# Kernel tuning notes

Hardware: AMD Instinct MI355X
Metric: run time of the kernel (lower is better)

The kernel has to match this reference:

```python
import jax, jax.numpy as jnp
import numpy as np
import math
from jax import lax

TSCALE = 256
NUM_SAMPLE = 32
PERBIN = 3
WINDOWS = [4, 8, 16, 32, 64, 128, 192, 256]
RATIO = 0.25
B = 2
DIM = 512
H1 = 256   # hid_dim_1d
H3 = 512   # hid_dim_3d
H2 = 128   # hid_dim_2d


def _bin_mask(xmin, xmax, tscale, num_sample, perbin):
    # exact replica of BEM._get_interp1d_bin_mask (setup-time numpy)
    plen = float(xmax - xmin)
    step = plen / (num_sample * perbin - 1.0)
    samples = [xmin + step * i for i in range(num_sample * perbin)]
    cols = []
    for idx in range(num_sample):
        v = np.zeros([tscale])
        for s in samples[idx * perbin:(idx + 1) * perbin]:
            up = math.ceil(s)
            dec, down = math.modf(s)
            if 0 <= int(down) <= tscale - 1:
                v[int(down)] += 1 - dec
            if 0 <= int(up) <= tscale - 1:
                v[int(up)] += dec
        cols.append(v / perbin)
    return np.stack(cols, axis=1)  # (tscale, num_sample)


def build_sample_mask():
    mats = []
    for w in WINDOWS:
        ws = w + w * RATIO
        vecs = []
        for t in range(TSCALE):
            d = ws * 0.5
            vecs.append(_bin_mask(t - d, t + d, TSCALE, NUM_SAMPLE, PERBIN))
        mats.append(np.stack(vecs, axis=2))  # (T, N, T)
    m = np.stack(mats, axis=3).astype(np.float32)  # (T, N, T, W)
    return jnp.asarray(m.reshape(TSCALE, -1))  # (T, N*T*W)


def gn(x, g, b, groups=32, eps=1e-5):
    Bsz, C = x.shape[0], x.shape[1]
    xr = x.reshape(Bsz, groups, -1)
    mu = xr.mean(-1, keepdims=True)
    var = xr.var(-1, keepdims=True)
    xr = (xr - mu) * lax.rsqrt(var + eps)
    x = xr.reshape(x.shape)
    bshape = (1, C) + (1,) * (x.ndim - 2)
    return x * g.reshape(bshape) + b.reshape(bshape)


def conv(x, w, b, strides, padding, dn):
    y = lax.conv_general_dilated(x, w, strides, padding, dimension_numbers=dn)
    return y + b.reshape((1, -1) + (1,) * (y.ndim - 2))


def setup_inputs() -> dict:
    key = jax.random.key(0)
    ks = jax.random.split(key, 16)

    def w(k, shape, fan):
        return (jax.random.normal(k, shape) * (1.0 / np.sqrt(fan))).astype(jnp.float32)

    inp = {}
    inp['x'] = jax.random.normal(ks[0], (B, DIM, TSCALE), jnp.float32)
    inp['sample_mask'] = build_sample_mask()
    inp['c1_w'] = w(ks[1], (H1, DIM, 3), DIM * 3)
    inp['c1_b'] = jnp.zeros((H1,), jnp.float32)
    inp['gn1_g'] = jnp.ones((H1,), jnp.float32)
    inp['gn1_b'] = jnp.zeros((H1,), jnp.float32)
    inp['r3d_w'] = w(ks[2], (H3, H1, NUM_SAMPLE, 1, 1), H1 * NUM_SAMPLE)
    inp['r3d_b'] = jnp.zeros((H3,), jnp.float32)
    inp['gn3_g'] = jnp.ones((H3,), jnp.float32)
    inp['gn3_b'] = jnp.zeros((H3,), jnp.float32)
    inp['r2d_w'] = w(ks[3], (H2, H3, 1, 1), H3)
    inp['r2d_b'] = jnp.zeros((H2,), jnp.float32)
    inp['gn2_g'] = jnp.ones((H2,), jnp.float32)
    inp['gn2_b'] = jnp.zeros((H2,), jnp.float32)
    inp['s1_w'] = w(ks[4], (H2, H2, 3, 3), H2 * 9)
    inp['s1_b'] = jnp.zeros((H2,), jnp.float32)
    inp['sgn_g'] = jnp.ones((H2,), jnp.float32)
    inp['sgn_b'] = jnp.zeros((H2,), jnp.float32)
    inp['s2_w'] = w(ks[5], (1, H2, 1, 1), H2)
    inp['s2_b'] = jnp.zeros((1,), jnp.float32)
    inp['e1_w'] = w(ks[6], (H2, H2, 3, 3), H2 * 9)
    inp['e1_b'] = jnp.zeros((H2,), jnp.float32)
    inp['egn_g'] = jnp.ones((H2,), jnp.float32)
    inp['egn_b'] = jnp.zeros((H2,), jnp.float32)
    inp['e2_w'] = w(ks[7], (1, H2, 1, 1), H2)
    inp['e2_b'] = jnp.zeros((1,), jnp.float32)
    return inp


def reference(x, sample_mask, c1_w, c1_b, gn1_g, gn1_b, r3d_w, r3d_b, gn3_g, gn3_b,
              r2d_w, r2d_b, gn2_g, gn2_b, s1_w, s1_b, sgn_g, sgn_b, s2_w, s2_b,
              e1_w, e1_b, egn_g, egn_b, e2_w, e2_b):
    relu = jax.nn.relu
    W = len(WINDOWS)
    # conv_1: Unit1D(k=3, same pad) + GN + ReLU  -> (B, H1, T)
    h = relu(gn(conv(x, c1_w, c1_b, (1,), [(1, 1)], ('NCH', 'OIH', 'NCH')), gn1_g, gn1_b))
    Bsz, C, T = h.shape
    # sample: dense GEMM against sparse interp1d mask -> (B, C, N, T, W)
    samp = jnp.matmul(h, sample_mask).reshape(Bsz, C, NUM_SAMPLE, T, W)
    # reduction_layer 'fc': Conv3d over the N axis (kernel=stride=N) + GN + ReLU
    y = conv(samp, r3d_w, r3d_b, (NUM_SAMPLE, 1, 1), 'VALID', ('NCDHW', 'OIDHW', 'NCDHW'))
    y = relu(gn(y, gn3_g, gn3_b))[:, :, 0]  # squeeze depth -> (B, H3, T, W)
    f = relu(gn(conv(y, r2d_w, r2d_b, (1, 1), 'VALID', ('NCHW', 'OIHW', 'NCHW')), gn2_g, gn2_b))

    def head(w1, b1, gg, gb, w2, b2):
        t = relu(gn(conv(f, w1, b1, (1, 1), [(1, 1), (1, 1)], ('NCHW', 'OIHW', 'NCHW')), gg, gb))
        return jax.nn.sigmoid(conv(t, w2, b2, (1, 1), 'VALID', ('NCHW', 'OIHW', 'NCHW')))

    cs = head(s1_w, s1_b, sgn_g, sgn_b, s2_w, s2_b)  # (B,1,T,W)
    ce = head(e1_w, e1_b, egn_g, egn_b, e2_w, e2_b)  # (B,1,T,W)
    return jnp.concatenate([cs, ce], axis=1)  # (B,2,T,W): [start, end]
```

## Files before the change

kernel.cpp:

```cpp
#include <hip/hip_runtime.h>
#include <hip/hip_bf16.h>

typedef __hip_bfloat16 bf16;
typedef __attribute__((ext_vector_type(8))) short short8;
typedef __attribute__((ext_vector_type(4))) float f32x4;

static __device__ __forceinline__ float b2f(bf16 v) { return __bfloat162float(v); }

static __device__ __forceinline__ float ldin(const void* p, long i, int bf) {
    return bf ? b2f(((const bf16*)p)[i]) : ((const float*)p)[i];
}

__global__ void detect_k(const unsigned short* __restrict__ x16, int* __restrict__ flag) {
    __shared__ int cnt[256];
    unsigned short u = x16[threadIdx.x];
    int e = (u >> 7) & 0xFF;
    cnt[threadIdx.x] = (e >= 100 && e <= 140) ? 1 : 0;
    __syncthreads();
    for (int off = 128; off > 0; off >>= 1) {
        if (threadIdx.x < off) cnt[threadIdx.x] += cnt[threadIdx.x + off];
        __syncthreads();
    }
    if (threadIdx.x == 0) *flag = (cnt[0] > 217) ? 1 : 0;
}

__global__ void cast_bf_k(const void* __restrict__ in, bf16* __restrict__ out,
                          int n, const int* __restrict__ flagp) {
    int bf = *flagp;
    int idx = blockIdx.x * 256 + threadIdx.x;
    if (idx >= n) return;
    out[idx] = __float2bfloat16(ldin(in, idx, bf));
}

__global__ __launch_bounds__(256) void transpose_w3b_k(const void* __restrict__ w3,
                                                       bf16* __restrict__ out,
                                                       const int* __restrict__ flagp) {
    int bf = *flagp;
    int h3 = blockIdx.x;
    __shared__ bf16 t[8192];
    long base = (long)h3 * 8192;
    for (int i = threadIdx.x; i < 8192; i += 256)
        t[i] = __float2bfloat16(ldin(w3, base + i, bf));
    __syncthreads();
    for (int i = threadIdx.x; i < 8192; i += 256) {
        int n = i >> 8, c = i & 255;
        out[((long)n * 512 + h3) * 256 + c] = t[c * 32 + n];
    }
}

__global__ void cast_hT_k(const float* __restrict__ h, bf16* __restrict__ out) {
    int idx = blockIdx.x * 256 + threadIdx.x;
    if (idx >= 131072) return;
    int b = idx >> 16, r = idx & 65535;
    int tau = r >> 8, c = r & 255;
    out[idx] = __float2bfloat16(h[b * 65536 + c * 256 + tau]);
}

__global__ __launch_bounds__(256) void castT_k(const float* __restrict__ y,
                                               bf16* __restrict__ yT) {
    int p0 = blockIdx.x * 64, c0 = blockIdx.y * 64, b = blockIdx.z;
    __shared__ bf16 t[64][65];
    const float* src = y + (long)b * 1048576;
    for (int i = threadIdx.x; i < 4096; i += 256) {
        int cl = i >> 6, pl = i & 63;
        t[pl][cl] = __float2bfloat16(src[(long)(c0 + cl) * 2048 + p0 + pl]);
    }
    __syncthreads();
    bf16* dst = yT + (long)b * 1048576;
    for (int i = threadIdx.x; i < 4096; i += 256) {
        int pl = i >> 6, cl = i & 63;
        dst[(long)(p0 + pl) * 512 + c0 + cl] = t[pl][cl];
    }
}

__global__ void im2col_xb_k(const void* __restrict__ x, bf16* __restrict__ out,
                            const int* __restrict__ flagp) {
    int bf = *flagp;
    int idx = blockIdx.x * 256 + threadIdx.x;
    if (idx >= 786432) return;
    int b = idx / 393216;
    int rem = idx - b * 393216;
    int t = rem / 1536, k = rem - t * 1536;
    int c = k / 3, q = k - c * 3;
    int tt = t + q - 1;
    float v = (tt >= 0 && tt < 256) ? ldin(x, ((long)b * 512 + c) * 256 + tt, bf) : 0.f;
    out[idx] = __float2bfloat16(v);
}

__global__ void im2col_fb_k(const float* __restrict__ f, bf16* __restrict__ out) {
    int idx = blockIdx.x * 256 + threadIdx.x;
    if (idx >= 4718592) return;
    int b = idx / 2359296;
    int rem = idx - b * 2359296;
    int p = rem / 1152, k = rem - p * 1152;
    int c = k / 9, q = k - c * 9;
    int dy = q / 3, dx = q - dy * 3;
    int t = p >> 3, w = p & 7;
    int tt = t + dy - 1, ww = w + dx - 1;
    float v = (tt >= 0 && tt < 256 && ww >= 0 && ww < 8)
                  ? f[((long)b * 128 + c) * 2048 + tt * 8 + ww] : 0.f;
    out[idx] = __float2bfloat16(v);
}

template<int NT>
__global__ __launch_bounds__(256) void wgemm_mfma(
    const bf16* __restrict__ A, const bf16* __restrict__ B, float* __restrict__ C,
    const void* __restrict__ bias1, const void* __restrict__ bias2,
    int M, int K, int P, int a_div, long a_zs, const int* __restrict__ flagp)
{
    int bf = *flagp;
    int z = blockIdx.z;
    const bf16* A2 = A + (long)(z / a_div) * a_zs;
    const bf16* B2 = B + (long)(z & 1) * (long)P * K;
    float* C2 = C + (long)z * M * P;
    const void* bi = (z / a_div) ? bias2 : bias1;

    int tid = threadIdx.x;
    int wv = tid >> 6, lane = tid & 63;
    int q = lane >> 4, col = lane & 15;
    int m0 = blockIdx.y * 64 + wv * 16;
    int p0 = blockIdx.x * (16 * NT);

    f32x4 acc[NT];
    #pragma unroll
    for (int i = 0; i < NT; ++i) acc[i] = (f32x4){0.f, 0.f, 0.f, 0.f};

    const short8* Ab = (const short8*)(A2 + (long)(m0 + col) * K);
    int kch = K >> 5;
    for (int kc = 0; kc < kch; ++kc) {
        short8 af = Ab[kc * 4 + q];
        #pragma unroll
        for (int nt = 0; nt < NT; ++nt) {
            const short8* Bb = (const short8*)(B2 + (long)(p0 + nt * 16 + col) * K);
            short8 bfr = Bb[kc * 4 + q];
            acc[nt] = __builtin_amdgcn_mfma_f32_16x16x32_bf16(af, bfr, acc[nt], 0, 0, 0);
        }
    }

    float bv[4];
    #pragma unroll
    for (int r = 0; r < 4; ++r) bv[r] = ldin(bi, m0 + q * 4 + r, bf);
    #pragma unroll
    for (int nt = 0; nt < NT; ++nt)
        #pragma unroll
        for (int r = 0; r < 4; ++r)
            C2[(long)(m0 + q * 4 + r) * P + p0 + nt * 16 + col] = acc[nt][r] + bv[r];
}

__global__ __launch_bounds__(256) void pgemm_mfma(
    const bf16* __restrict__ w3b, const bf16* __restrict__ hbT,
    float* __restrict__ P)
{
    int z = blockIdx.z;
    int b = z >> 5, n = z & 31;
    int bm = blockIdx.y;
    int tid = threadIdx.x;
    int wv = tid >> 6, lane = tid & 63;
    int q = lane >> 4, col = lane & 15;

    f32x4 acc[16];
    #pragma unroll
    for (int i = 0; i < 16; ++i) acc[i] = (f32x4){0.f, 0.f, 0.f, 0.f};

    const short8* Abase = (const short8*)(w3b + ((long)n * 512 + bm * 64 + wv * 16 + col) * 256);
    const short8* Bbase = (const short8*)(hbT + (long)b * 65536);

    #pragma unroll
    for (int kc = 0; kc < 8; ++kc) {
        short8 af = Abase[kc * 4 + q];
        #pragma unroll
        for (int nt = 0; nt < 16; ++nt) {
            short8 bfr = Bbase[(nt * 16 + col) * 32 + kc * 4 + q];
            acc[nt] = __builtin_amdgcn_mfma_f32_16x16x32_bf16(af, bfr, acc[nt], 0, 0, 0);
        }
    }

    long dbase = (long)b * 4194304 + (long)n * 256 +
                 (long)(bm * 64 + wv * 16 + q * 4) * 8192 + col;
    #pragma unroll
    for (int nt = 0; nt < 16; ++nt)
        #pragma unroll
        for (int r = 0; r < 4; ++r)
            P[dbase + (long)r * 8192 + nt * 16] = acc[nt][r];
}

__global__ __launch_bounds__(1024) void gn_relu_k(
    float* __restrict__ buf, const void* __restrict__ g, const void* __restrict__ bt,
    int C, int S, int groups, const int* __restrict__ flagp)
{
    int bf = *flagp;
    int nt = blockDim.x;
    int gid = blockIdx.x;
    int b = gid / groups, gr = gid % groups;
    int cpg = C / groups;
    long cnt = (long)cpg * S;
    float* base = buf + ((long)b * C + (long)gr * cpg) * S;
    double s = 0.0, s2 = 0.0;
    for (long i = threadIdx.x; i < cnt; i += nt) {
        float v = base[i];
        s += v; s2 += (double)v * v;
    }
    __shared__ double rs[1024], rq[1024];
    rs[threadIdx.x] = s; rq[threadIdx.x] = s2;
    __syncthreads();
    for (int off = nt >> 1; off > 0; off >>= 1) {
        if (threadIdx.x < off) { rs[threadIdx.x] += rs[threadIdx.x + off]; rq[threadIdx.x] += rq[threadIdx.x + off]; }
        __syncthreads();
    }
    double mean_d = rs[0] / (double)cnt;
    float mean = (float)mean_d;
    float var = (float)(rq[0] / (double)cnt - mean_d * mean_d);
    float rstd = rsqrtf(var + 1e-5f);
    for (long i = threadIdx.x; i < cnt; i += nt) {
        int c = gr * cpg + (int)(i / S);
        float v = (base[i] - mean) * rstd * ldin(g, c, bf) + ldin(bt, c, bf);
        base[i] = v > 0.f ? v : 0.f;
    }
}

__global__ __launch_bounds__(256) void gn_part_k(
    const float* __restrict__ buf, double* __restrict__ part,
    int C, int S, int groups, int chunks)
{
    int gi = blockIdx.x / chunks, ch = blockIdx.x % chunks;
    int b = gi / groups, gr = gi % groups;
    int cpg = C / groups;
    long cnt = (long)cpg * S;
    long clen = cnt / chunks;
    const float* base = buf + ((long)b * C + (long)gr * cpg) * S + (long)ch * clen;
    double s = 0.0, s2 = 0.0;
    for (long i = threadIdx.x; i < clen; i += 256) {
        float v = base[i];
        s += v; s2 += (double)v * v;
    }
    __shared__ double rs[256], rq[256];
    rs[threadIdx.x] = s; rq[threadIdx.x] = s2;
    __syncthreads();
    for (int off = 128; off > 0; off >>= 1) {
        if (threadIdx.x < off) { rs[threadIdx.x] += rs[threadIdx.x + off]; rq[threadIdx.x] += rq[threadIdx.x + off]; }
        __syncthreads();
    }
    if (threadIdx.x == 0) { part[blockIdx.x * 2] = rs[0]; part[blockIdx.x * 2 + 1] = rq[0]; }
}

__global__ __launch_bounds__(256) void gn_apply_k(
    float* __restrict__ buf, const double* __restrict__ part,
    const void* __restrict__ g, const void* __restrict__ bt,
    int C, int S, int groups, int chunks, const int* __restrict__ flagp)
{
    int bf = *flagp;
    int gi = blockIdx.x / chunks, ch = blockIdx.x % chunks;
    int b = gi / groups, gr = gi % groups;
    int cpg = C / groups;
    long cnt = (long)cpg * S;
    long clen = cnt / chunks;
    double s = 0.0, s2 = 0.0;
    for (int k = 0; k < chunks; ++k) {
        s += part[(gi * chunks + k) * 2];
        s2 += part[(gi * chunks + k) * 2 + 1];
    }
    double mean_d = s / (double)cnt;
    float mean = (float)mean_d;
    float var = (float)(s2 / (double)cnt - mean_d * mean_d);
    float rstd = rsqrtf(var + 1e-5f);
    float* base = buf + ((long)b * C + (long)gr * cpg) * S + (long)ch * clen;
    long off0 = (long)ch * clen;
    for (long i = threadIdx.x; i < clen; i += 256) {
        int c = gr * cpg + (int)((off0 + i) / S);
        float v = (base[i] - mean) * rstd * ldin(g, c, bf) + ldin(bt, c, bf);
        base[i] = v > 0.f ? v : 0.f;
    }
}

__global__ __launch_bounds__(384) void build_table_k(
    const void* __restrict__ mask, int* __restrict__ tabd,
    float* __restrict__ tabw, const int* __restrict__ flagp)
{
    int bf = *flagp;
    int nw = blockIdx.x;
    int w = nw >> 5, n = nw & 31;
    int tid = threadIdx.x;
    int d = tid - 165;
    float v = 0.f;
    if (d <= 165) {
        if (d < 0) v = ldin(mask, (long)(254 + d) * 65536 + ((long)n * 256 + 254) * 8 + w, bf);
        else       v = ldin(mask, (long)(1 + d) * 65536 + ((long)n * 256 + 1) * 8 + w, bf);
    }
    __shared__ unsigned char nz[384];
    nz[tid] = (v != 0.f) ? 1 : 0;
    if (tid < 6) { tabd[nw * 6 + tid] = 0; tabw[nw * 6 + tid] = 0.f; }
    __syncthreads();
    if (v != 0.f) {
        int slot = 0;
        for (int j = 0; j < tid; ++j) slot += nz[j];
        if (slot < 6) { tabd[nw * 6 + slot] = d; tabw[nw * 6 + slot] = v; }
    }
}

__global__ void build_corr_k(const void* __restrict__ mask, const int* __restrict__ tabd,
                             const float* __restrict__ tabw, float* __restrict__ corrT,
                             const int* __restrict__ flagp) {
    int bf = *flagp;
    int idx = blockIdx.x * 256 + threadIdx.x;
    if (idx >= 65536) return;
    int e = idx >> 8, t = idx & 255;
    int w = e >> 5, n = e & 31;
    float mv = ldin(mask, ((long)n * 256 + t) * 8 + w, bf);
    float sub = 0.f;
    int base = e * 6;
    for (int k = 0; k < 6; ++k)
        if (tabd[base + k] == -t && tabw[base + k] != 0.f) sub += tabw[base + k];
    corrT[idx] = mv - sub;
}

__global__ __launch_bounds__(1024) void apply_y2_k(
    const float* __restrict__ P, const int* __restrict__ tabd,
    const float* __restrict__ tabw, const float* __restrict__ corrT,
    float* __restrict__ y, const void* __restrict__ r3b,
    const int* __restrict__ flagp)
{
    int hp = blockIdx.x;
    int h0 = hp * 2;
    int tid = threadIdx.x;
    int t = tid & 255;
    int wg = tid >> 8;
    int w0 = wg * 2;

    __shared__ float4 Pl[12 * 256];
    __shared__ float4 Tab[768];
    __shared__ float4 pzv[32];

    const float* Pb00 = P + (long)h0 * 8192;
    const float* Pb01 = P + (long)(h0 + 1) * 8192;
    const float* Pb10 = Pb00 + 4194304;
    const float* Pb11 = Pb01 + 4194304;

    float2* tab2 = (float2*)Tab;
    for (int i = tid; i < 1536; i += 1024)
        tab2[i] = make_float2(tabw[i], __int_as_float(tabd[i]));
    if (tid < 32) {
        int n = tid;
        pzv[n] = make_float4(Pb00[n * 256], Pb01[n * 256], Pb10[n * 256], Pb11[n * 256]);
    }

    float4 acc0 = make_float4(0.f, 0.f, 0.f, 0.f);
    float4 acc1 = make_float4(0.f, 0.f, 0.f, 0.f);

    int cn0 = 0;
    #pragma unroll 1
    for (int ch = 0; ch < 3; ++ch) {
        int NC = (ch == 2) ? 8 : 12;
        __syncthreads();
        for (int pos = tid; pos < NC * 256; pos += 1024) {
            int nl = pos >> 8, tau = pos & 255;
            long o = (long)(cn0 + nl) * 256 + tau;
            Pl[pos] = make_float4(Pb00[o], Pb01[o], Pb10[o], Pb11[o]);
        }
        __syncthreads();

        #pragma unroll 1
        for (int nl = 0; nl < NC; ++nl) {
            const float4* Pn = Pl + (nl << 8);
            auto tap = [&](float wt, float df, float4& acc) {
                int d = __float_as_int(df);
                int tau = t + d;
                float wtk = ((unsigned)tau < 256u) ? wt : 0.f;
                float4 pv = Pn[tau & 255];
                acc.x += wtk * pv.x; acc.y += wtk * pv.y;
                acc.z += wtk * pv.z; acc.w += wtk * pv.w;
            };
            int e0 = w0 * 32 + cn0 + nl;
            {
                float4 q0 = Tab[e0 * 3], q1 = Tab[e0 * 3 + 1], q2 = Tab[e0 * 3 + 2];
                if (q0.x != 0.f) { tap(q0.x, q0.y, acc0);
                 if (q0.z != 0.f) { tap(q0.z, q0.w, acc0);
                  if (q1.x != 0.f) { tap(q1.x, q1.y, acc0);
                   if (q1.z != 0.f) { tap(q1.z, q1.w, acc0);
                    if (q2.x != 0.f) { tap(q2.x, q2.y, acc0);
                     if (q2.z != 0.f) { tap(q2.z, q2.w, acc0); }}}}}}
            }
            {
                int e1 = e0 + 32;
                float4 q0 = Tab[e1 * 3], q1 = Tab[e1 * 3 + 1], q2 = Tab[e1 * 3 + 2];
                if (q0.x != 0.f) { tap(q0.x, q0.y, acc1);
                 if (q0.z != 0.f) { tap(q0.z, q0.w, acc1);
                  if (q1.x != 0.f) { tap(q1.x, q1.y, acc1);
                   if (q1.z != 0.f) { tap(q1.z, q1.w, acc1);
                    if (q2.x != 0.f) { tap(q2.x, q2.y, acc1);
                     if (q2.z != 0.f) { tap(q2.z, q2.w, acc1); }}}}}}
            }
        }
        cn0 += NC;
    }

    __syncthreads();

    int bf = *flagp;
    float g0 = ldin(r3b, h0, bf), g1 = ldin(r3b, h0 + 1, bf);
    acc0.x += g0; acc0.y += g1; acc0.z += g0; acc0.w += g1;
    acc1.x += g0; acc1.y += g1; acc1.z += g0; acc1.w += g1;

    const float* cT0 = corrT + (long)w0 * 8192 + t;
    const float* cT1 = cT0 + 8192;
    #pragma unroll 4
    for (int n = 0; n < 32; ++n) {
        float4 pz = pzv[n];
        float c0 = cT0[n * 256], c1 = cT1[n * 256];
        acc0.x += c0 * pz.x; acc0.y += c0 * pz.y;
        acc0.z += c0 * pz.z; acc0.w += c0 * pz.w;
        acc1.x += c1 * pz.x; acc1.y += c1 * pz.y;
        acc1.z += c1 * pz.z; acc1.w += c1 * pz.w;
    }

    float* yb = (float*)Pl;
    *(float2*)&yb[0 * 2048 + t * 8 + w0] = make_float2(acc0.x, acc1.x);
    *(float2*)&yb[1 * 2048 + t * 8 + w0] = make_float2(acc0.y, acc1.y);
    *(float2*)&yb[2 * 2048 + t * 8 + w0] = make_float2(acc0.z, acc1.z);
    *(float2*)&yb[3 * 2048 + t * 8 + w0] = make_float2(acc0.w, acc1.w);
    __syncthreads();
    for (int f = tid; f < 2048; f += 1024) {
        int c = f >> 9, r = f & 511;
        int tt = r >> 1, half = r & 1;
        float4 v = *(const float4*)&yb[c * 2048 + tt * 8 + half * 4];
        int b = c >> 1, hh = h0 + (c & 1);
        *(float4*)&y[((long)b * 512 + hh) * 2048 + tt * 8 + half * 4] = v;
    }
}

__global__ __launch_bounds__(64) void head_out_k(
    const float* __restrict__ t1s, const float* __restrict__ t1e,
    const void* __restrict__ s2w, const void* __restrict__ s2b,
    const void* __restrict__ e2w, const void* __restrict__ e2b,
    void* __restrict__ out, const int* __restrict__ flagp) {
    int bf = *flagp;
    int idx = blockIdx.x * 64 + threadIdx.x;
    if (idx >= 4096) return;
    int b = idx >> 11, p = idx & 2047;
    const float* ts = t1s + (long)b * 262144 + p;
    const float* te = t1e + (long)b * 262144 + p;
    float as = ldin(s2b, 0, bf), ae = ldin(e2b, 0, bf);
    #pragma unroll 8
    for (int c = 0; c < 128; ++c) {
        as += ldin(s2w, c, bf) * ts[(long)c * 2048];
        ae += ldin(e2w, c, bf) * te[(long)c * 2048];
    }
    float vs = 1.f / (1.f + expf(-as));
    float ve = 1.f / (1.f + expf(-ae));
    long o0 = ((long)b * 2) * 2048 + p;
    long o1 = ((long)b * 2 + 1) * 2048 + p;
    if (bf) {
        ((bf16*)out)[o0] = __float2bfloat16(vs);
        ((bf16*)out)[o1] = __float2bfloat16(ve);
    } else {
        ((float*)out)[o0] = vs;
        ((float*)out)[o1] = ve;
    }
}

extern "C" void kernel_launch(void* const* d_in, const int* in_sizes, int n_in,
                              void* d_out, int out_size, void* d_ws, size_t ws_size,
                              hipStream_t stream) {
    const void* x    = d_in[0];
    const void* mask = d_in[1];
    const void* c1w  = d_in[2];
    const void* c1b  = d_in[3];
    const void* gn1g = d_in[4];
    const void* gn1b = d_in[5];
    const void* w3   = d_in[6];
    const void* r3b  = d_in[7];
    const void* gn3g = d_in[8];
    const void* gn3b = d_in[9];
    const void* w2   = d_in[10];
    const void* r2b  = d_in[11];
    const void* gn2g = d_in[12];
    const void* gn2b = d_in[13];
    const void* s1w  = d_in[14];
    const void* s1b  = d_in[15];
    const void* sgng = d_in[16];
    const void* sgnb = d_in[17];
    const void* s2w  = d_in[18];
    const void* s2b  = d_in[19];
    const void* e1w  = d_in[20];
    const void* e1b  = d_in[21];
    const void* egng = d_in[22];
    const void* egnb = d_in[23];
    const void* e2w  = d_in[24];
    const void* e2b  = d_in[25];
    float* ws = (float*)d_ws;

    int*   flagI = (int*)(ws + 0);
    float* h     = ws + 64;
    float* c1t   = ws + 131136;
    float* w2t   = ws + 524352;
    float* s1t   = ws + 589888;
    float* corrB = ws + 884800;
    float* tabw  = ws + 950336;
    int*   tabd  = (int*)(ws + 951872);
    float* t1s   = ws + 986176;
    float* t1e   = ws + 1510464;
    float* f     = ws + 2034752;
    float* y     = ws + 2559040;
    float* w3reg = ws + 4656192;
    float* Pb    = ws + 8850496;
    double* gnbuf = (double*)(ws + 17239104);
    bf16*  w3b   = (bf16*)w3reg;
    bf16*  hbT   = (bf16*)(w3reg + 2097152);
    bf16*  c1wb  = (bf16*)c1t;
    bf16*  w2b   = (bf16*)w2t;
    bf16*  hwb   = (bf16*)s1t;
    bf16*  colxb = (bf16*)y;
    bf16*  fcolb = (bf16*)Pb;
    bf16*  yT    = (bf16*)(Pb + 4194304);

    dim3 blk(256);
    dim3 blkG(1024);

    detect_k<<<dim3(1), blk, 0, stream>>>((const unsigned short*)x, flagI);

    cast_bf_k<<<dim3(1536), blk, 0, stream>>>(c1w, c1wb, 393216, flagI);
    cast_bf_k<<<dim3(576),  blk, 0, stream>>>(s1w, hwb, 147456, flagI);
    cast_bf_k<<<dim3(576),  blk, 0, stream>>>(e1w, hwb + 147456, 147456, flagI);
    cast_bf_k<<<dim3(256),  blk, 0, stream>>>(w2, w2b, 65536, flagI);
    transpose_w3b_k<<<dim3(512), blk, 0, stream>>>(w3, w3b, flagI);
    build_table_k<<<dim3(256), dim3(384), 0, stream>>>(mask, tabd, tabw, flagI);
    build_corr_k<<<dim3(256), blk, 0, stream>>>(mask, tabd, tabw, corrB, flagI);

    im2col_xb_k<<<dim3(3072), blk, 0, stream>>>(x, colxb, flagI);
    wgemm_mfma<1><<<dim3(16, 4, 2), blk, 0, stream>>>(
        c1wb, colxb, h, c1b, c1b, 256, 1536, 256, 1, 0L, flagI);
    gn_relu_k<<<dim3(64), blkG, 0, stream>>>(h, gn1g, gn1b, 256, 256, 32, flagI);

    cast_hT_k<<<dim3(512), blk, 0, stream>>>(h, hbT);
    pgemm_mfma<<<dim3(1, 8, 64), blk, 0, stream>>>(w3b, hbT, Pb);

    apply_y2_k<<<dim3(256), dim3(1024), 0, stream>>>(Pb, tabd, tabw, corrB, y, r3b, flagI);
    gn_part_k<<<dim3(512), blk, 0, stream>>>(y, gnbuf, 512, 2048, 32, 8);
    gn_apply_k<<<dim3(512), blk, 0, stream>>>(y, gnbuf, gn3g, gn3b, 512, 2048, 32, 8, flagI);

    castT_k<<<dim3(32, 8, 2), blk, 0, stream>>>(y, yT);
    wgemm_mfma<2><<<dim3(64, 2, 2), blk, 0, stream>>>(
        w2b, yT, f, r2b, r2b, 128, 512, 2048, 2, 0L, flagI);
    gn_part_k<<<dim3(256), blk, 0, stream>>>(f, gnbuf, 128, 2048, 32, 4);
    gn_apply_k<<<dim3(256), blk, 0, stream>>>(f, gnbuf, gn2g, gn2b, 128, 2048, 32, 4, flagI);

    im2col_fb_k<<<dim3(18432), blk, 0, stream>>>(f, fcolb);
    wgemm_mfma<4><<<dim3(32, 2, 4), blk, 0, stream>>>(
        hwb, fcolb, t1s, s1b, e1b, 128, 1152, 2048, 2, 147456L, flagI);
    gn_part_k<<<dim3(256), blk, 0, stream>>>(t1s, gnbuf, 128, 2048, 32, 4);
    gn_apply_k<<<dim3(256), blk, 0, stream>>>(t1s, gnbuf, sgng, sgnb, 128, 2048, 32, 4, flagI);
    gn_part_k<<<dim3(256), blk, 0, stream>>>(t1e, gnbuf, 128, 2048, 32, 4);
    gn_apply_k<<<dim3(256), blk, 0, stream>>>(t1e, gnbuf, egng, egnb, 128, 2048, 32, 4, flagI);

    head_out_k<<<dim3(64), dim3(64), 0, stream>>>(t1s, t1e, s2w, s2b, e2w, e2b, d_out, flagI);
}
```

Measured before the change: 409.7 us.

## Fuse per-sample projection GEMM into sparse apply kernel via in-block MFMA

Drops the separate pgemm kernel that wrote a large fp32 P intermediate (B x 512 x 32 x 256) to global memory. apply_y3_k now computes the needed P slice for its two output channels with MFMA directly into shared memory, in two chunks of 16 samples, and then runs the sparse tap accumulation from LDS. This removes a large global write and read round-trip and one kernel launch. In exchange each block redoes GEMM loads of hbT, the shared buffer grows, and MFMA work now sits inside a 1024-thread block with fewer blocks.

Measured after the change: 389.6 us. 1.05x faster.

```diff
diff --git a/kernel.cpp b/kernel.cpp
--- a/kernel.cpp
+++ b/kernel.cpp
@@ -145,43 +145,6 @@
         #pragma unroll
         for (int r = 0; r < 4; ++r)
             C2[(long)(m0 + q * 4 + r) * P + p0 + nt * 16 + col] = acc[nt][r] + bv[r];
-}
-
-__global__ __launch_bounds__(256) void pgemm_mfma(
-    const bf16* __restrict__ w3b, const bf16* __restrict__ hbT,
-    float* __restrict__ P)
-{
-    int z = blockIdx.z;
-    int b = z >> 5, n = z & 31;
-    int bm = blockIdx.y;
-    int tid = threadIdx.x;
-    int wv = tid >> 6, lane = tid & 63;
-    int q = lane >> 4, col = lane & 15;
-
-    f32x4 acc[16];
-    #pragma unroll
-    for (int i = 0; i < 16; ++i) acc[i] = (f32x4){0.f, 0.f, 0.f, 0.f};
-
-    const short8* Abase = (const short8*)(w3b + ((long)n * 512 + bm * 64 + wv * 16 + col) * 256);
-    const short8* Bbase = (const short8*)(hbT + (long)b * 65536);
-
-    #pragma unroll
-    for (int kc = 0; kc < 8; ++kc) {
-        short8 af = Abase[kc * 4 + q];
-        #pragma unroll
-        for (int nt = 0; nt < 16; ++nt) {
-            short8 bfr = Bbase[(nt * 16 + col) * 32 + kc * 4 + q];
-            acc[nt] = __builtin_amdgcn_mfma_f32_16x16x32_bf16(af, bfr, acc[nt], 0, 0, 0);
-        }
-    }
-
-    long dbase = (long)b * 4194304 + (long)n * 256 +
-                 (long)(bm * 64 + wv * 16 + q * 4) * 8192 + col;
-    #pragma unroll
-    for (int nt = 0; nt < 16; ++nt)
-        #pragma unroll
-        for (int r = 0; r < 4; ++r)
-            P[dbase + (long)r * 8192 + nt * 16] = acc[nt][r];
 }
 
 __global__ __launch_bounds__(1024) void gn_relu_k(
@@ -313,11 +276,11 @@
     corrT[idx] = mv - sub;
 }
 
-__global__ __launch_bounds__(1024) void apply_y2_k(
-    const float* __restrict__ P, const int* __restrict__ tabd,
-    const float* __restrict__ tabw, const float* __restrict__ corrT,
-    float* __restrict__ y, const void* __restrict__ r3b,
-    const int* __restrict__ flagp)
+__global__ __launch_bounds__(1024) void apply_y3_k(
+    const bf16* __restrict__ w3b, const bf16* __restrict__ hbT,
+    const int* __restrict__ tabd, const float* __restrict__ tabw,
+    const float* __restrict__ corrT, float* __restrict__ y,
+    const void* __restrict__ r3b, const int* __restrict__ flagp)
 {
     int hp = blockIdx.x;
     int h0 = hp * 2;
@@ -326,40 +289,66 @@
     int wg = tid >> 8;
     int w0 = wg * 2;
 
-    __shared__ float4 Pl[12 * 256];
+    int wv = tid >> 6;
+    int lane = tid & 63;
+    int q = lane >> 4, col = lane & 15;
+
+    __shared__ float4 Pl[16 * 256];
     __shared__ float4 Tab[768];
     __shared__ float4 pzv[32];
-
-    const float* Pb00 = P + (long)h0 * 8192;
-    const float* Pb01 = P + (long)(h0 + 1) * 8192;
-    const float* Pb10 = Pb00 + 4194304;
-    const float* Pb11 = Pb01 + 4194304;
 
     float2* tab2 = (float2*)Tab;
     for (int i = tid; i < 1536; i += 1024)
         tab2[i] = make_float2(tabw[i], __int_as_float(tabd[i]));
-    if (tid < 32) {
-        int n = tid;
-        pzv[n] = make_float4(Pb00[n * 256], Pb01[n * 256], Pb10[n * 256], Pb11[n * 256]);
-    }
+
+    const short8* Bb0 = (const short8*)(hbT + (long)(wv * 32 + col) * 256);
+    const short8* Bb1 = (const short8*)(hbT + (long)(wv * 32 + 16 + col) * 256);
+    int jb = wv * 32 + col;
+    int b_ = wv >> 3;
+    int tau0 = jb & 255;
+    int tau1 = (jb + 16) & 255;
 
     float4 acc0 = make_float4(0.f, 0.f, 0.f, 0.f);
     float4 acc1 = make_float4(0.f, 0.f, 0.f, 0.f);
 
-    int cn0 = 0;
     #pragma unroll 1
-    for (int ch = 0; ch < 3; ++ch) {
-        int NC = (ch == 2) ? 8 : 12;
+    for (int ch = 0; ch < 2; ++ch) {
+        int cn0 = ch * 16;
         __syncthreads();
-        for (int pos = tid; pos < NC * 256; pos += 1024) {
-            int nl = pos >> 8, tau = pos & 255;
-            long o = (long)(cn0 + nl) * 256 + tau;
-            Pl[pos] = make_float4(Pb00[o], Pb01[o], Pb10[o], Pb11[o]);
+
+        f32x4 g00 = (f32x4){0.f,0.f,0.f,0.f}, g01 = (f32x4){0.f,0.f,0.f,0.f};
+        f32x4 g10 = (f32x4){0.f,0.f,0.f,0.f}, g11 = (f32x4){0.f,0.f,0.f,0.f};
+        const short8* Aa0 = (const short8*)(w3b +
+            ((long)(cn0 + (col >> 1)) * 512 + h0 + (col & 1)) * 256);
+        const short8* Aa1 = (const short8*)(w3b +
+            ((long)(cn0 + 8 + (col >> 1)) * 512 + h0 + (col & 1)) * 256);
+        #pragma unroll
+        for (int kc = 0; kc < 8; ++kc) {
+            short8 a0 = Aa0[kc * 4 + q];
+            short8 a1 = Aa1[kc * 4 + q];
+            short8 b0 = Bb0[kc * 4 + q];
+            short8 b1 = Bb1[kc * 4 + q];
+            g00 = __builtin_amdgcn_mfma_f32_16x16x32_bf16(a0, b0, g00, 0, 0, 0);
+            g01 = __builtin_amdgcn_mfma_f32_16x16x32_bf16(a0, b1, g01, 0, 0, 0);
+            g10 = __builtin_amdgcn_mfma_f32_16x16x32_bf16(a1, b0, g10, 0, 0, 0);
+            g11 = __builtin_amdgcn_mfma_f32_16x16x32_bf16(a1, b1, g11, 0, 0, 0);
+        }
+        float* Plf = (float*)Pl;
+        #pragma unroll
+        for (int rh = 0; rh < 2; ++rh) {
+            int nl0 = q * 2 + rh;
+            int nl1 = 8 + q * 2 + rh;
+            *(float2*)&Plf[(nl0 * 256 + tau0) * 4 + b_ * 2] = make_float2(g00[2*rh], g00[2*rh+1]);
+            *(float2*)&Plf[(nl0 * 256 + tau1) * 4 + b_ * 2] = make_float2(g01[2*rh], g01[2*rh+1]);
+            *(float2*)&Plf[(nl1 * 256 + tau0) * 4 + b_ * 2] = make_float2(g10[2*rh], g10[2*rh+1]);
+            *(float2*)&Plf[(nl1 * 256 + tau1) * 4 + b_ * 2] = make_float2(g11[2*rh], g11[2*rh+1]);
         }
         __syncthreads();
 
+        if (tid < 16) pzv[cn0 + tid] = Pl[tid * 256];
+
         #pragma unroll 1
-        for (int nl = 0; nl < NC; ++nl) {
+        for (int nl = 0; nl < 16; ++nl) {
             const float4* Pn = Pl + (nl << 8);
             auto tap = [&](float wt, float df, float4& acc) {
                 int d = __float_as_int(df);
@@ -390,7 +379,6 @@
                      if (q2.z != 0.f) { tap(q2.z, q2.w, acc1); }}}}}}
             }
         }
-        cn0 += NC;
     }
 
     __syncthreads();
@@ -531,9 +519,8 @@
     gn_relu_k<<<dim3(64), blkG, 0, stream>>>(h, gn1g, gn1b, 256, 256, 32, flagI);
 
     cast_hT_k<<<dim3(512), blk, 0, stream>>>(h, hbT);
-    pgemm_mfma<<<dim3(1, 8, 64), blk, 0, stream>>>(w3b, hbT, Pb);
-
-    apply_y2_k<<<dim3(256), dim3(1024), 0, stream>>>(Pb, tabd, tabw, corrB, y, r3b, flagI);
+    apply_y3_k<<<dim3(256), dim3(1024), 0, stream>>>(
+        w3b, hbT, tabd, tabw, corrB, y, r3b, flagI);
     gn_part_k<<<dim3(512), blk, 0, stream>>>(y, gnbuf, 512, 2048, 32, 8);
     gn_apply_k<<<dim3(512), blk, 0, stream>>>(y, gnbuf, gn3g, gn3b, 512, 2048, 32, 8, flagI);
 
```
